# Optimization experiments

Hardware: AMD Instinct MI355X
Metric: run time of the kernel (lower is better)

The kernel has to match this reference:

```python
import jax, jax.numpy as jnp
import numpy as np

B, T, D, H = 4, 2048, 1024, 16
HS = D // H  # head_size = 64
EPS = 1e-5


def _layernorm(x, g, b):
    mu = jnp.mean(x, axis=-1, keepdims=True)
    var = jnp.var(x, axis=-1, keepdims=True)
    return (x - mu) * jax.lax.rsqrt(var + EPS) * g + b


def setup_inputs() -> dict:
    key = jax.random.key(0)
    ks = jax.random.split(key, 12)
    s = lambda fan_in: 1.0 / np.sqrt(fan_in)
    return {
        "x": jax.random.normal(ks[0], (B, T, D), dtype=jnp.float32),
        # per-head projections, stacked: (H, D, HS)
        "Wq": jax.random.uniform(ks[1], (H, D, HS), jnp.float32, -s(D), s(D)),
        "Wk": jax.random.uniform(ks[2], (H, D, HS), jnp.float32, -s(D), s(D)),
        "Wv": jax.random.uniform(ks[3], (H, D, HS), jnp.float32, -s(D), s(D)),
        "Wo": jax.random.uniform(ks[4], (D, D), jnp.float32, -s(D), s(D)),
        "bo": jax.random.uniform(ks[5], (D,), jnp.float32, -s(D), s(D)),
        "W1": jax.random.uniform(ks[6], (D, 4 * D), jnp.float32, -s(D), s(D)),
        "b1": jax.random.uniform(ks[7], (4 * D,), jnp.float32, -s(D), s(D)),
        "W2": jax.random.uniform(ks[8], (4 * D, D), jnp.float32, -s(4 * D), s(4 * D)),
        "b2": jax.random.uniform(ks[9], (D,), jnp.float32, -s(4 * D), s(4 * D)),
        "g1": jnp.ones((D,), jnp.float32),
        "be1": jnp.zeros((D,), jnp.float32),
        "g2": jnp.ones((D,), jnp.float32),
        "be2": jnp.zeros((D,), jnp.float32),
    }


def reference(x, Wq, Wk, Wv, Wo, bo, W1, b1, W2, b2, g1, be1, g2, be2):
    # --- self-attention sublayer (pre-LN) ---
    h = _layernorm(x, g1, be1)                       # (B,T,D)
    q = jnp.einsum('btd,hds->bhts', h, Wq)           # (B,H,T,HS)
    k = jnp.einsum('btd,hds->bhts', h, Wk)
    v = jnp.einsum('btd,hds->bhts', h, Wv)
    scores = jnp.einsum('bhts,bhus->bhtu', q, k) * (HS ** -0.5)  # (B,H,T,T)
    causal = jnp.tril(jnp.ones((T, T), dtype=bool))
    scores = jnp.where(causal, scores, -jnp.inf)
    w = jax.nn.softmax(scores, axis=-1)
    attn = jnp.einsum('bhtu,bhus->bhts', w, v)       # (B,H,T,HS)
    attn = attn.transpose(0, 2, 1, 3).reshape(B, T, D)  # concat heads
    x = x + attn @ Wo + bo
    # --- feed-forward sublayer (pre-LN) ---
    h2 = _layernorm(x, g2, be2)
    x = x + jax.nn.relu(h2 @ W1 + b1) @ W2 + b2
    return x
```

## Files before the change

### kernel.cpp

```cpp
#include <hip/hip_runtime.h>
#include <hip/hip_bf16.h>
#include <cstddef>

#define B_ 4
#define T_ 2048
#define D_ 1024
#define H_ 16
#define HS_ 64
#define QS_ 3072

typedef short short8 __attribute__((ext_vector_type(8)));
typedef float f32x4 __attribute__((ext_vector_type(4)));

__device__ __forceinline__ unsigned short f2b(float x) {
    __hip_bfloat16 b = __float2bfloat16(x);
    return *reinterpret_cast<unsigned short*>(&b);
}

__device__ __forceinline__ void gload_lds16(const void* g, void* l) {
    __builtin_amdgcn_global_load_lds((const __attribute__((address_space(1))) void*)g,
                                     (__attribute__((address_space(3))) void*)l, 16, 0, 0);
}

__global__ __launch_bounds__(256) void ln_kernel(const float* __restrict__ X,
                                                 const float* __restrict__ g,
                                                 const float* __restrict__ be,
                                                 unsigned short* __restrict__ O)
{
    const int row = blockIdx.x;
    const int tid = threadIdx.x;
    const float* xr = X + (size_t)row * D_;
    float4 xv = *reinterpret_cast<const float4*>(xr + tid * 4);
    float s  = xv.x + xv.y + xv.z + xv.w;
    float s2 = xv.x * xv.x + xv.y * xv.y + xv.z * xv.z + xv.w * xv.w;
#pragma unroll
    for (int off = 32; off > 0; off >>= 1) {
        s  += __shfl_xor(s,  off);
        s2 += __shfl_xor(s2, off);
    }
    __shared__ float red[8];
    const int wid = tid >> 6, lane = tid & 63;
    if (lane == 0) { red[wid * 2] = s; red[wid * 2 + 1] = s2; }
    __syncthreads();
    s  = red[0] + red[2] + red[4] + red[6];
    s2 = red[1] + red[3] + red[5] + red[7];
    const float mu  = s * (1.0f / D_);
    const float var = s2 * (1.0f / D_) - mu * mu;
    const float r   = rsqrtf(var + 1e-5f);
    float4 gv = *reinterpret_cast<const float4*>(g  + tid * 4);
    float4 bv = *reinterpret_cast<const float4*>(be + tid * 4);
    ushort4 ov;
    ov.x = f2b((xv.x - mu) * r * gv.x + bv.x);
    ov.y = f2b((xv.y - mu) * r * gv.y + bv.y);
    ov.z = f2b((xv.z - mu) * r * gv.z + bv.z);
    ov.w = f2b((xv.w - mu) * r * gv.w + bv.w);
    *reinterpret_cast<ushort4*>(O + (size_t)row * D_ + tid * 4) = ov;
}

__global__ __launch_bounds__(256) void transpose_all(const float* __restrict__ Wq,
                                                     const float* __restrict__ Wk,
                                                     const float* __restrict__ Wv,
                                                     const float* __restrict__ Wo,
                                                     const float* __restrict__ W1,
                                                     const float* __restrict__ W2,
                                                     unsigned short* __restrict__ Wtqkv,
                                                     unsigned short* __restrict__ Wto,
                                                     unsigned short* __restrict__ Wt1,
                                                     unsigned short* __restrict__ Wt2)
{
    __shared__ float tile[32][33];
    const int tx = threadIdx.x & 31, ty = threadIdx.x >> 5;
    int s = blockIdx.x;

    if (s < 3072) {
        const float* in = (s < 1024) ? Wq : (s < 2048) ? Wk : Wv;
        const int noff = (s < 1024) ? 0 : (s < 2048) ? D_ : 2 * D_;
        s &= 1023;
        const int bn = (s & 31) * 32, bk = (s >> 5) * 32;
        const int head = bn >> 6, s0 = bn & 63;
#pragma unroll
        for (int i = 0; i < 32; i += 8)
            tile[ty + i][tx] = in[(size_t)head * D_ * HS_ + (size_t)(bk + ty + i) * HS_ + s0 + tx];
        __syncthreads();
#pragma unroll
        for (int i = 0; i < 32; i += 8)
            Wtqkv[(size_t)(noff + bn + ty + i) * D_ + bk + tx] = f2b(tile[tx][ty + i]);
        return;
    }
    s -= 3072;
    const float* in; unsigned short* out; int K, N, bn, bk;
    if (s < 1024)      { in = Wo; out = Wto; K = D_;     N = D_;     bn = (s & 31) * 32;  bk = (s >> 5) * 32; }
    else if (s < 5120) { s -= 1024; in = W1; out = Wt1; K = D_;     N = 4 * D_; bn = (s & 127) * 32; bk = (s >> 7) * 32; }
    else               { s -= 5120; in = W2; out = Wt2; K = 4 * D_; N = D_;     bn = (s & 31) * 32;  bk = (s >> 5) * 32; }
#pragma unroll
    for (int i = 0; i < 32; i += 8)
        tile[ty + i][tx] = in[(size_t)(bk + ty + i) * N + bn + tx];
    __syncthreads();
#pragma unroll
    for (int i = 0; i < 32; i += 8)
        out[(size_t)(bn + ty + i) * K + bk + tx] = f2b(tile[tx][ty + i]);
}

template<bool BIAS, bool RELU, bool RESID, bool OUT_BF16, bool SCALEQ>
__global__ __launch_bounds__(512, 1) void gemm_sq(const unsigned short* __restrict__ A,
                                                  const unsigned short* __restrict__ Bt,
                                                  const float* __restrict__ bias,
                                                  const float* __restrict__ resid,
                                                  float* __restrict__ Cf,
                                                  unsigned short* __restrict__ Cb,
                                                  int M, int N, int K)
{
    constexpr int BUFS = 16384 + 16384;
    __shared__ __attribute__((aligned(128))) unsigned short lds[2 * BUFS];

    const int tid = threadIdx.x, l = tid & 63, w = tid >> 6;
    const int wRow = w >> 2, wCol = w & 3;
    const int lr = l & 15, lq = l >> 4;

    const int gx = gridDim.x;
    const int nwg = gx * (int)gridDim.y;
    const int orig = (int)blockIdx.y * gx + (int)blockIdx.x;
    const int xcd = orig & 7, lo = orig >> 3;
    const int q8 = nwg >> 3, r8 = nwg & 7;
    const int wg = (xcd < r8 ? xcd * (q8 + 1) : r8 * (q8 + 1) + (xcd - r8) * q8) + lo;
    const int bm = wg / gx, bn = wg % gx;

    const int nt = K >> 6;

    auto ISSUE_HALF = [&](int t, int half) {
        const size_t kof = (size_t)t * 64;
        const int buf = t & 1;
        const unsigned short* src = (half < 2) ? A : Bt;
        const int rb = ((half < 2) ? bm : bn) * 256 + (half & 1) * 128;
        const int lb = buf * BUFS + ((half >= 2) ? 16384 : 0) + (half & 1) * 128 * 64;
#pragma unroll
        for (int p = 0; p < 2; ++p) {
            const int j = p * 512 + tid;
            const int row = j >> 3, ci = j & 7;
            gload_lds16(src + (size_t)(rb + row) * K + kof + ((ci ^ (row & 7)) * 8),
                        &lds[lb + j * 8]);
        }
    };

    f32x4 acc[8][4];
#pragma unroll
    for (int i = 0; i < 8; ++i)
#pragma unroll
        for (int j = 0; j < 4; ++j) acc[i][j] = (f32x4){0.f, 0.f, 0.f, 0.f};

    short8 af[4][2], bf[4][2];
    const int swz = lr & 7;

#pragma unroll
    for (int h = 0; h < 4; ++h) ISSUE_HALF(0, h);

    for (int t = 0; t < nt; ++t) {
        const unsigned short* As = &lds[(t & 1) * BUFS];
        const unsigned short* Bs = As + 16384;
        const bool more = (t + 1 < nt);

        asm volatile("s_waitcnt vmcnt(0)" ::: "memory");
        __builtin_amdgcn_s_barrier();

        if (more) ISSUE_HALF(t + 1, 0);
#pragma unroll
        for (int mi = 0; mi < 4; ++mi) {
            const int row = wRow * 128 + mi * 16 + lr;
#pragma unroll
            for (int ks = 0; ks < 2; ++ks)
                af[mi][ks] = *reinterpret_cast<const short8*>(&As[row * 64 + (((ks * 4 + lq) ^ swz) * 8)]);
        }
#pragma unroll
        for (int nj = 0; nj < 2; ++nj) {
            const int rowB = wCol * 64 + nj * 16 + lr;
#pragma unroll
            for (int ks = 0; ks < 2; ++ks)
                bf[nj][ks] = *reinterpret_cast<const short8*>(&Bs[rowB * 64 + (((ks * 4 + lq) ^ swz) * 8)]);
        }
        asm volatile("s_waitcnt lgkmcnt(0)" ::: "memory");
        __builtin_amdgcn_sched_barrier(0);
        __builtin_amdgcn_s_setprio(1);
#pragma unroll
        for (int mi = 0; mi < 4; ++mi)
#pragma unroll
            for (int nj = 0; nj < 2; ++nj)
#pragma unroll
                for (int ks = 0; ks < 2; ++ks)
                    acc[mi][nj] = __builtin_amdgcn_mfma_f32_16x16x32_bf16(af[mi][ks], bf[nj][ks], acc[mi][nj], 0, 0, 0);
        __builtin_amdgcn_s_setprio(0);

        if (more) ISSUE_HALF(t + 1, 1);
#pragma unroll
        for (int nj = 2; nj < 4; ++nj) {
            const int rowB = wCol * 64 + nj * 16 + lr;
#pragma unroll
            for (int ks = 0; ks < 2; ++ks)
                bf[nj][ks] = *reinterpret_cast<const short8*>(&Bs[rowB * 64 + (((ks * 4 + lq) ^ swz) * 8)]);
        }
        asm volatile("s_waitcnt lgkmcnt(0)" ::: "memory");
        __builtin_amdgcn_sched_barrier(0);
        __builtin_amdgcn_s_setprio(1);
#pragma unroll
        for (int mi = 0; mi < 4; ++mi)
#pragma unroll
            for (int nj = 2; nj < 4; ++nj)
#pragma unroll
                for (int ks = 0; ks < 2; ++ks)
                    acc[mi][nj] = __builtin_amdgcn_mfma_f32_16x16x32_bf16(af[mi][ks], bf[nj][ks], acc[mi][nj], 0, 0, 0);
        __builtin_amdgcn_s_setprio(0);

        if (more) { ISSUE_HALF(t + 1, 2); ISSUE_HALF(t + 1, 3); }
#pragma unroll
        for (int mi = 0; mi < 4; ++mi) {
            const int row = wRow * 128 + (4 + mi) * 16 + lr;
#pragma unroll
            for (int ks = 0; ks < 2; ++ks)
                af[mi][ks] = *reinterpret_cast<const short8*>(&As[row * 64 + (((ks * 4 + lq) ^ swz) * 8)]);
        }
        asm volatile("s_waitcnt lgkmcnt(0)" ::: "memory");
        __builtin_amdgcn_sched_barrier(0);
        __builtin_amdgcn_s_setprio(1);
#pragma unroll
        for (int mi = 0; mi < 4; ++mi)
#pragma unroll
            for (int nj = 0; nj < 2; ++nj)
#pragma unroll
                for (int ks = 0; ks < 2; ++ks)
                    acc[4 + mi][nj] = __builtin_amdgcn_mfma_f32_16x16x32_bf16(af[mi][ks], bf[nj][ks], acc[4 + mi][nj], 0, 0, 0);
        __builtin_amdgcn_s_setprio(0);

        __builtin_amdgcn_s_setprio(1);
#pragma unroll
        for (int mi = 0; mi < 4; ++mi)
#pragma unroll
            for (int nj = 2; nj < 4; ++nj)
#pragma unroll
                for (int ks = 0; ks < 2; ++ks)
                    acc[4 + mi][nj] = __builtin_amdgcn_mfma_f32_16x16x32_bf16(af[mi][ks], bf[nj][ks], acc[4 + mi][nj], 0, 0, 0);
        __builtin_amdgcn_s_setprio(0);
    }

    const int m0 = bm * 256 + wRow * 128;
    const int n0 = bn * 256 + wCol * 64;
#pragma unroll
    for (int nf = 0; nf < 4; ++nf) {
        const int col = n0 + nf * 16 + lr;
        const float bv = BIAS ? bias[col] : 0.0f;
#pragma unroll
        for (int mf = 0; mf < 8; ++mf) {
#pragma unroll
            for (int r = 0; r < 4; ++r) {
                const int row = m0 + mf * 16 + lq * 4 + r;
                float c = acc[mf][nf][r] + bv;
                if (RELU) c = fmaxf(c, 0.0f);
                if (RESID) c += resid[(size_t)row * N + col];
                if (SCALEQ) { if (col < D_) c *= 0.18033688f; }
                if (OUT_BF16) Cb[(size_t)row * N + col] = f2b(c);
                else          Cf[(size_t)row * N + col] = c;
            }
        }
    }
}

template<bool MASKED>
__device__ __forceinline__ void attn_chunk(
    const unsigned short* __restrict__ ksb,
    const unsigned short (* __restrict__ vsb)[72],
    unsigned short (* __restrict__ psw)[72],
    const short8* aq, f32x4* o,
    int lr, int lq, int wl)
{
    const short8 vone = {0x3F80, 0x3F80, 0x3F80, 0x3F80, 0x3F80, 0x3F80, 0x3F80, 0x3F80};
    f32x4 s[4];
#pragma unroll
    for (int kb = 0; kb < 4; ++kb) s[kb] = (f32x4){0.f, 0.f, 0.f, 0.f};
    __builtin_amdgcn_s_setprio(1);
#pragma unroll
    for (int kb = 0; kb < 4; ++kb) {
        if (MASKED && kb > wl) continue;
        const int row = kb * 16 + lr;
        const int sw = row & 7;
#pragma unroll
        for (int ks = 0; ks < 2; ++ks) {
            const int ch = (ks * 4 + lq) ^ sw;
            const short8 bk = *reinterpret_cast<const short8*>(&ksb[row * 64 + ch * 8]);
            s[kb] = __builtin_amdgcn_mfma_f32_16x16x32_bf16(aq[ks], bk, s[kb], 0, 0, 0);
        }
    }
    __builtin_amdgcn_s_setprio(0);

#pragma unroll
    for (int r = 0; r < 4; ++r) {
        const int qloc = wl * 16 + lq * 4 + r;
        float p[4];
#pragma unroll
        for (int kb = 0; kb < 4; ++kb) {
            const bool msk = MASKED && (kb * 16 + lr > qloc);
            p[kb] = msk ? 0.0f : exp2f(s[kb][r]);
        }
        const unsigned int w0 = (unsigned int)f2b(p[0]) | ((unsigned int)f2b(p[1]) << 16);
        const unsigned int w1 = (unsigned int)f2b(p[2]) | ((unsigned int)f2b(p[3]) << 16);
        uint2 pk; pk.x = w0; pk.y = w1;
        *reinterpret_cast<uint2*>(&psw[lq * 4 + r][lr * 4]) = pk;
    }
    asm volatile("s_waitcnt lgkmcnt(0)" ::: "memory");
    __builtin_amdgcn_s_setprio(1);
#pragma unroll
    for (int ks = 0; ks < 2; ++ks) {
        const short8 pa = *reinterpret_cast<const short8*>(&psw[lr][ks * 32 + lq * 8]);
#pragma unroll
        for (int df = 0; df < 4; ++df) {
            const short8 vb = *reinterpret_cast<const short8*>(&vsb[df * 16 + lr][ks * 32 + lq * 8]);
            o[df] = __builtin_amdgcn_mfma_f32_16x16x32_bf16(pa, vb, o[df], 0, 0, 0);
        }
        o[4] = __builtin_amdgcn_mfma_f32_16x16x32_bf16(pa, vone, o[4], 0, 0, 0);
    }
    __builtin_amdgcn_s_setprio(0);
}

__global__ __launch_bounds__(512, 4) void attn_mfma(const unsigned short* __restrict__ QKV,
                                                    unsigned short* __restrict__ Og)
{
    __shared__ __attribute__((aligned(128))) unsigned short Ks[2][64 * 64];
    __shared__ __attribute__((aligned(16)))  unsigned short Vs[2][64][72];
    __shared__ __attribute__((aligned(16)))  unsigned short Ps[8][16][72];

    const int NQT = T_ / 128;
    const int px = blockIdx.x;
    const int qtA = px, qtB = NQT - 1 - px;
    const int h = blockIdx.y, b = blockIdx.z;
    const int tid = threadIdx.x, w = tid >> 6, l = tid & 63;
    const int wl = w & 3, qsub = w >> 2;
    const int lr = l & 15, lq = l >> 4;
    const size_t base = (size_t)b * T_ * QS_ + h * HS_;

    short8 aqA[2], aqB[2];
    {
        const int qrl = qsub * 64 + wl * 16 + lr;
        const unsigned short* pA = QKV + base + (size_t)(qtA * 128 + qrl) * QS_;
        const unsigned short* pB = QKV + base + (size_t)(qtB * 128 + qrl) * QS_;
        aqA[0] = *reinterpret_cast<const short8*>(pA + lq * 8);
        aqA[1] = *reinterpret_cast<const short8*>(pA + 32 + lq * 8);
        aqB[0] = *reinterpret_cast<const short8*>(pB + lq * 8);
        aqB[1] = *reinterpret_cast<const short8*>(pB + 32 + lq * 8);
    }

    const unsigned short* Kg = QKV + D_;
    const unsigned short* Vg = QKV + 2 * D_;

    auto stage = [&](int c, int bf) {
        const int kbase = c * 64;
        {
            const int row = tid >> 3;
            const int c8 = ((tid & 7) ^ (row & 7)) * 8;
            gload_lds16(Kg + base + (size_t)(kbase + row) * QS_ + c8,
                        &Ks[bf][tid * 8]);
        }
        {
            const int vkey = tid & 63, vd0 = (tid >> 6) * 8;
            const int jkey = (vkey & 15) * 4 + (vkey >> 4);
            const unsigned short* vsrc = Vg + base + (size_t)(kbase + vkey) * QS_ + vd0;
            short8 v0 = *reinterpret_cast<const short8*>(vsrc);
#pragma unroll
            for (int jj = 0; jj < 8; ++jj) Vs[bf][vd0 + jj][jkey] = (unsigned short)v0[jj];
        }
    };

    stage(0, 0);
    __syncthreads();

    unsigned short (*psw)[72] = Ps[w];

    f32x4 oA[5], oB[5];
#pragma unroll
    for (int df = 0; df < 5; ++df) {
        oA[df] = (f32x4){0.f, 0.f, 0.f, 0.f};
        oB[df] = (f32x4){0.f, 0.f, 0.f, 0.f};
    }

    const int qminw = qsub * 64 + wl * 16;
    const int qmaxw = qminw + 15;

    const int nch = 2 * qtB + 2;
    int bf = 0;
    for (int c = 0; c < nch; ++c) {
        if (c + 1 < nch) stage(c + 1, bf ^ 1);
        const int relA = c * 64 - qtA * 128;
        const int relB = c * 64 - qtB * 128;
        if (relA <= qmaxw) {
            if (relA + 63 <= qminw)
                attn_chunk<false>(&Ks[bf][0], Vs[bf], psw, aqA, oA, lr, lq, wl);
            else
                attn_chunk<true>(&Ks[bf][0], Vs[bf], psw, aqA, oA, lr, lq, wl);
        }
        if (relB <= qmaxw) {
            if (relB + 63 <= qminw)
                attn_chunk<false>(&Ks[bf][0], Vs[bf], psw, aqB, oB, lr, lq, wl);
            else
                attn_chunk<true>(&Ks[bf][0], Vs[bf], psw, aqB, oB, lr, lq, wl);
        }
        if (c + 1 < nch) __syncthreads();
        bf ^= 1;
    }

    const size_t obase = (size_t)b * T_ * D_ + h * HS_;
#pragma unroll
    for (int r = 0; r < 4; ++r) {
        const float invA = 1.0f / oA[4][r];
        const float invB = 1.0f / oB[4][r];
        const int qrl = qsub * 64 + wl * 16 + lq * 4 + r;
        unsigned short* orowA = Og + obase + (size_t)(qtA * 128 + qrl) * D_;
        unsigned short* orowB = Og + obase + (size_t)(qtB * 128 + qrl) * D_;
#pragma unroll
        for (int df = 0; df < 4; ++df) {
            orowA[df * 16 + lr] = f2b(oA[df][r] * invA);
            orowB[df * 16 + lr] = f2b(oB[df][r] * invB);
        }
    }
}

extern "C" void kernel_launch(void* const* d_in, const int* in_sizes, int n_in,
                              void* d_out, int out_size, void* d_ws, size_t ws_size,
                              hipStream_t stream)
{
    const float* x   = (const float*)d_in[0];
    const float* Wq  = (const float*)d_in[1];
    const float* Wk  = (const float*)d_in[2];
    const float* Wv  = (const float*)d_in[3];
    const float* Wo  = (const float*)d_in[4];
    const float* bo  = (const float*)d_in[5];
    const float* W1  = (const float*)d_in[6];
    const float* b1  = (const float*)d_in[7];
    const float* W2  = (const float*)d_in[8];
    const float* b2  = (const float*)d_in[9];
    const float* g1  = (const float*)d_in[10];
    const float* be1 = (const float*)d_in[11];
    const float* g2  = (const float*)d_in[12];
    const float* be2 = (const float*)d_in[13];
    float* out = (float*)d_out;

    unsigned short* ws = (unsigned short*)d_ws;
    const size_t NT = (size_t)B_ * T_;
    unsigned short* hb    = ws;
    unsigned short* QKVb  = hb + NT * D_;
    unsigned short* Ab    = QKVb + NT * 3 * D_;
    unsigned short* f1    = QKVb;
    unsigned short* Wtqkv = Ab + NT * D_;
    unsigned short* Wto   = Wtqkv + (size_t)3 * D_ * D_;
    unsigned short* Wt1   = Wto + (size_t)D_ * D_;
    unsigned short* Wt2   = Wt1 + (size_t)4 * D_ * D_;

    dim3 b256(256), b512(512);

    transpose_all<<<dim3(12288), b256, 0, stream>>>(Wq, Wk, Wv, Wo, W1, W2,
                                                    Wtqkv, Wto, Wt1, Wt2);

    ln_kernel<<<NT, b256, 0, stream>>>(x, g1, be1, hb);

    gemm_sq<false, false, false, true, true><<<dim3(3 * D_ / 256, NT / 256), b512, 0, stream>>>(
        hb, Wtqkv, nullptr, nullptr, nullptr, QKVb, (int)NT, 3 * D_, D_);

    attn_mfma<<<dim3(T_ / 256, H_, B_), b512, 0, stream>>>(QKVb, Ab);

    gemm_sq<true, false, true, false, false><<<dim3(D_ / 256, NT / 256), b512, 0, stream>>>(
        Ab, Wto, bo, x, out, nullptr, (int)NT, D_, D_);

    ln_kernel<<<NT, b256, 0, stream>>>(out, g2, be2, hb);

    gemm_sq<true, true, false, true, false><<<dim3(4 * D_ / 256, NT / 256), b512, 0, stream>>>(
        hb, Wt1, b1, nullptr, nullptr, f1, (int)NT, 4 * D_, D_);

    gemm_sq<true, false, true, false, false><<<dim3(D_ / 256, NT / 256), b512, 0, stream>>>(
        f1, Wt2, b2, out, out, nullptr, (int)NT, D_, 4 * D_);
}
```

Baseline: 377.3 us.

## Add 128x256-tile GEMM variant with XCD remap for QKV, Wo and W2 GEMMs

Adds a second GEMM kernel that uses 128x256 output tiles, triple-buffered LDS loads and an XCD-aware remapping of workgroup IDs. The QKV, output-projection and FFN-down GEMMs now use it, while FFN-up keeps the 256x256 kernel. Halving the M tile doubles the number of workgroups for the N=1024 GEMMs, which gives better CU occupancy on the 256-CU part, and the remap keeps neighbouring tiles on the same XCD for L2 reuse. The cost is lower arithmetic intensity per tile and more global traffic for B.

```diff
diff --git a/kernel.cpp b/kernel.cpp
--- a/kernel.cpp
+++ b/kernel.cpp
@@ -248,6 +248,138 @@
         const float bv = BIAS ? bias[col] : 0.0f;
 #pragma unroll
         for (int mf = 0; mf < 8; ++mf) {
+#pragma unroll
+            for (int r = 0; r < 4; ++r) {
+                const int row = m0 + mf * 16 + lq * 4 + r;
+                float c = acc[mf][nf][r] + bv;
+                if (RELU) c = fmaxf(c, 0.0f);
+                if (RESID) c += resid[(size_t)row * N + col];
+                if (SCALEQ) { if (col < D_) c *= 0.18033688f; }
+                if (OUT_BF16) Cb[(size_t)row * N + col] = f2b(c);
+                else          Cf[(size_t)row * N + col] = c;
+            }
+        }
+    }
+}
+
+template<bool BIAS, bool RELU, bool RESID, bool OUT_BF16, bool SCALEQ>
+__global__ __launch_bounds__(512, 1) void gemm_sq2(const unsigned short* __restrict__ A,
+                                                   const unsigned short* __restrict__ Bt,
+                                                   const float* __restrict__ bias,
+                                                   const float* __restrict__ resid,
+                                                   float* __restrict__ Cf,
+                                                   unsigned short* __restrict__ Cb,
+                                                   int M, int N, int K)
+{
+    constexpr int BUFS = 8192 + 16384;
+    __shared__ __attribute__((aligned(128))) unsigned short lds[3 * BUFS];
+
+    const int tid = threadIdx.x, l = tid & 63, w = tid >> 6;
+    const int wRow = w >> 2, wCol = w & 3;
+    const int lr = l & 15, lq = l >> 4;
+
+    const int gx = gridDim.x;
+    const int nwg = gx * (int)gridDim.y;
+    const int orig = (int)blockIdx.y * gx + (int)blockIdx.x;
+    const int xcd = orig & 7, lo = orig >> 3;
+    const int q8 = nwg >> 3, r8 = nwg & 7;
+    const int wg = (xcd < r8 ? xcd * (q8 + 1) : r8 * (q8 + 1) + (xcd - r8) * q8) + lo;
+    const int bm = wg / gx, bn = wg % gx;
+
+    const int nt = K >> 6;
+
+    auto ISSUE = [&](int t, int buf) {
+        const size_t kof = (size_t)t * 64;
+#pragma unroll
+        for (int p = 0; p < 2; ++p) {
+            const int j = p * 512 + tid;
+            const int row = j >> 3, ci = j & 7;
+            gload_lds16(A + (size_t)(bm * 128 + row) * K + kof + ((ci ^ (row & 7)) * 8),
+                        &lds[buf * BUFS + j * 8]);
+        }
+#pragma unroll
+        for (int p = 0; p < 4; ++p) {
+            const int j = p * 512 + tid;
+            const int row = j >> 3, ci = j & 7;
+            gload_lds16(Bt + (size_t)(bn * 256 + row) * K + kof + ((ci ^ (row & 7)) * 8),
+                        &lds[buf * BUFS + 8192 + j * 8]);
+        }
+    };
+
+    f32x4 acc[4][4];
+#pragma unroll
+    for (int i = 0; i < 4; ++i)
+#pragma unroll
+        for (int j = 0; j < 4; ++j) acc[i][j] = (f32x4){0.f, 0.f, 0.f, 0.f};
+
+    short8 af[2][2], bf[4][2];
+    const int swz = lr & 7;
+
+    ISSUE(0, 0);
+    ISSUE(1, 1);
+
+    for (int t = 0; t < nt; ++t) {
+        const unsigned short* As = &lds[(t % 3) * BUFS];
+        const unsigned short* Bs = As + 8192;
+        if (t + 1 < nt) asm volatile("s_waitcnt vmcnt(6)" ::: "memory");
+        else            asm volatile("s_waitcnt vmcnt(0)" ::: "memory");
+        __builtin_amdgcn_s_barrier();
+        if (t + 2 < nt) ISSUE(t + 2, (t + 2) % 3);
+
+#pragma unroll
+        for (int mi = 0; mi < 2; ++mi) {
+            const int row = wRow * 64 + mi * 16 + lr;
+#pragma unroll
+            for (int ks = 0; ks < 2; ++ks)
+                af[mi][ks] = *reinterpret_cast<const short8*>(&As[row * 64 + (((ks * 4 + lq) ^ swz) * 8)]);
+        }
+#pragma unroll
+        for (int nj = 0; nj < 4; ++nj) {
+            const int rowB = wCol * 64 + nj * 16 + lr;
+#pragma unroll
+            for (int ks = 0; ks < 2; ++ks)
+                bf[nj][ks] = *reinterpret_cast<const short8*>(&Bs[rowB * 64 + (((ks * 4 + lq) ^ swz) * 8)]);
+        }
+        asm volatile("s_waitcnt lgkmcnt(0)" ::: "memory");
+        __builtin_amdgcn_sched_barrier(0);
+        __builtin_amdgcn_s_setprio(1);
+#pragma unroll
+        for (int mi = 0; mi < 2; ++mi)
+#pragma unroll
+            for (int nj = 0; nj < 4; ++nj)
+#pragma unroll
+                for (int ks = 0; ks < 2; ++ks)
+                    acc[mi][nj] = __builtin_amdgcn_mfma_f32_16x16x32_bf16(af[mi][ks], bf[nj][ks], acc[mi][nj], 0, 0, 0);
+        __builtin_amdgcn_s_setprio(0);
+
+#pragma unroll
+        for (int mi = 0; mi < 2; ++mi) {
+            const int row = wRow * 64 + (2 + mi) * 16 + lr;
+#pragma unroll
+            for (int ks = 0; ks < 2; ++ks)
+                af[mi][ks] = *reinterpret_cast<const short8*>(&As[row * 64 + (((ks * 4 + lq) ^ swz) * 8)]);
+        }
+        asm volatile("s_waitcnt lgkmcnt(0)" ::: "memory");
+        __builtin_amdgcn_sched_barrier(0);
+        __builtin_amdgcn_s_setprio(1);
+#pragma unroll
+        for (int mi = 0; mi < 2; ++mi)
+#pragma unroll
+            for (int nj = 0; nj < 4; ++nj)
+#pragma unroll
+                for (int ks = 0; ks < 2; ++ks)
+                    acc[2 + mi][nj] = __builtin_amdgcn_mfma_f32_16x16x32_bf16(af[mi][ks], bf[nj][ks], acc[2 + mi][nj], 0, 0, 0);
+        __builtin_amdgcn_s_setprio(0);
+    }
+
+    const int m0 = bm * 128 + wRow * 64;
+    const int n0 = bn * 256 + wCol * 64;
+#pragma unroll
+    for (int nf = 0; nf < 4; ++nf) {
+        const int col = n0 + nf * 16 + lr;
+        const float bv = BIAS ? bias[col] : 0.0f;
+#pragma unroll
+        for (int mf = 0; mf < 4; ++mf) {
 #pragma unroll
             for (int r = 0; r < 4; ++r) {
                 const int row = m0 + mf * 16 + lq * 4 + r;
@@ -457,12 +589,12 @@
 
     ln_kernel<<<NT, b256, 0, stream>>>(x, g1, be1, hb);
 
-    gemm_sq<false, false, false, true, true><<<dim3(3 * D_ / 256, NT / 256), b512, 0, stream>>>(
+    gemm_sq2<false, false, false, true, true><<<dim3(3 * D_ / 256, NT / 128), b512, 0, stream>>>(
         hb, Wtqkv, nullptr, nullptr, nullptr, QKVb, (int)NT, 3 * D_, D_);
 
     attn_mfma<<<dim3(T_ / 256, H_, B_), b512, 0, stream>>>(QKVb, Ab);
 
-    gemm_sq<true, false, true, false, false><<<dim3(D_ / 256, NT / 256), b512, 0, stream>>>(
+    gemm_sq2<true, false, true, false, false><<<dim3(D_ / 256, NT / 128), b512, 0, stream>>>(
         Ab, Wto, bo, x, out, nullptr, (int)NT, D_, D_);
 
     ln_kernel<<<NT, b256, 0, stream>>>(out, g2, be2, hb);
@@ -470,6 +602,6 @@
     gemm_sq<true, true, false, true, false><<<dim3(4 * D_ / 256, NT / 256), b512, 0, stream>>>(
         hb, Wt1, b1, nullptr, nullptr, f1, (int)NT, 4 * D_, D_);
 
-    gemm_sq<true, false, true, false, false><<<dim3(D_ / 256, NT / 256), b512, 0, stream>>>(
+    gemm_sq2<true, false, true, false, false><<<dim3(D_ / 256, NT / 128), b512, 0, stream>>>(
         f1, Wt2, b2, out, out, nullptr, (int)NT, D_, 4 * D_);
 }
```

Measured after the change: 342.7 us. 1.1x faster.
